# Kernel tuning notes

Hardware: AMD Instinct MI355X
Metric: run time of the kernel (lower is better)

Reference implementation:

```python
import jax, jax.numpy as jnp
import numpy as np

B, L, NW, H, HID, E, NL, DL = 32, 1024, 512, 768, 384, 4, 12, 128


def setup_inputs() -> dict:
    key = jax.random.key(0)
    ks = jax.random.split(key, 16)
    f = lambda k, s: jax.random.normal(k, s, dtype=jnp.float32) * 0.02
    z = lambda s: jnp.zeros(s, jnp.float32)
    return {
        "token_embs": jax.random.normal(ks[0], (B, L, H), dtype=jnp.float32),
        "word_maps": jnp.sort(jax.random.randint(ks[1], (B, L), 0, NW), axis=-1),
        "lang_ids": jax.random.randint(ks[2], (B,), 0, NL),
        # BiLSTM params (PyTorch gate order i,f,g,o packed along dim 0)
        "Wih_f": f(ks[3], (4 * HID, H)), "Whh_f": f(ks[4], (4 * HID, HID)),
        "bih_f": z((4 * HID,)), "bhh_f": z((4 * HID,)),
        "Wih_b": f(ks[5], (4 * HID, H)), "Whh_b": f(ks[6], (4 * HID, HID)),
        "bih_b": z((4 * HID,)), "bhh_b": z((4 * HID,)),
        "proj_W": f(ks[7], (H, 2 * HID)), "proj_b": z((H,)),
        "lang_table": f(ks[8], (NL, DL)),
        "gate_W1": f(ks[9], (H, H + DL)), "gate_b1": z((H,)),
        "gate_W2": f(ks[10], (E, H)), "gate_b2": z((E,)),
        # stacked expert heads: row i is expert i's (H,1) linear
        "ef_W": f(ks[11], (E, H)), "ef_b": z((E,)),
        "ed_W": f(ks[12], (E, H)), "ed_b": z((E,)),
    }


def _seg_mean(embs, wmap):
    # embs: [L, H], wmap: [L] -> [NW, H] per-word mean of subword embeddings
    sums = jax.ops.segment_sum(embs, wmap, num_segments=NW)
    cnt = jax.ops.segment_sum(jnp.ones(embs.shape[:1], embs.dtype), wmap, num_segments=NW)
    return sums / jnp.maximum(cnt, 1.0)[:, None]


def _lstm(x, Wih, Whh, bih, bhh, reverse):
    # x: [B, T, H] -> hidden states [B, T, HID]; gate order i,f,g,o
    def step(carry, xg):
        h, c = carry
        g = xg + h @ Whh.T + bhh
        i, fg, gg, o = jnp.split(g, 4, axis=-1)
        c = jax.nn.sigmoid(fg) * c + jax.nn.sigmoid(i) * jnp.tanh(gg)
        h = jax.nn.sigmoid(o) * jnp.tanh(c)
        return (h, c), h
    xg = jnp.swapaxes(x @ Wih.T + bih, 0, 1)  # [T, B, 4*HID], input proj hoisted
    init = (jnp.zeros((x.shape[0], Whh.shape[1]), x.dtype),) * 2
    _, hs = jax.lax.scan(step, init, xg, reverse=reverse)
    return jnp.swapaxes(hs, 0, 1)


def reference(token_embs, word_maps, lang_ids, Wih_f, Whh_f, bih_f, bhh_f,
              Wih_b, Whh_b, bih_b, bhh_b, proj_W, proj_b, lang_table,
              gate_W1, gate_b1, gate_W2, gate_b2, ef_W, ef_b, ed_W, ed_b):
    # subword -> word segment-mean pooling, batched
    word_embs = jax.vmap(_seg_mean)(token_embs, word_maps)          # [B, NW, H]
    hf = _lstm(word_embs, Wih_f, Whh_f, bih_f, bhh_f, False)        # [B, NW, HID]
    hb = _lstm(word_embs, Wih_b, Whh_b, bih_b, bhh_b, True)         # [B, NW, HID]
    seq = jnp.concatenate([hf, hb], axis=-1) @ proj_W.T + proj_b    # [B, NW, H]
    # dropout omitted (eval mode)
    gate_in = jnp.concatenate([token_embs[:, 0], lang_table[lang_ids]], axis=-1)  # [B, H+DL]
    gate = jax.nn.softmax(
        jax.nn.relu(gate_in @ gate_W1.T + gate_b1) @ gate_W2.T + gate_b2, axis=-1)  # [B, E]
    fix = jnp.einsum('bwe,be->bw', seq @ ef_W.T + ef_b, gate)       # [B, NW]
    dur = jnp.einsum('bwe,be->bw', seq @ ed_W.T + ed_b, gate)       # [B, NW]
    return (fix, dur)
```

## Files before the change

### kernel.cpp

```cpp
#include <hip/hip_runtime.h>
#include <stdint.h>

#define BB 32
#define LL 1024
#define NW 512
#define HH 768
#define HID 384
#define G4 1536
#define EE 4
#define DLL 128
#define GIN 896
#define CWG 12
#define WGC 32
#define HPAD 392

typedef __attribute__((ext_vector_type(8))) short short8;
typedef __attribute__((ext_vector_type(4))) float f32x4;
typedef __attribute__((ext_vector_type(2))) float f32x2;

__device__ __forceinline__ float bf2f(short s){
  union { unsigned int u; float f; } v; v.u = ((unsigned int)(unsigned short)s) << 16; return v.f;
}
__device__ __forceinline__ short f2bf(float f){
  union { float f; unsigned int u; } v; v.f = f;
  unsigned int r = v.u + 0x7fffu + ((v.u >> 16) & 1u);
  return (short)(r >> 16);
}
__device__ __forceinline__ float sigm(float x){ return 1.f / (1.f + __expf(-x)); }

__device__ __forceinline__ void gload16(const void* g, void* l){
  __builtin_amdgcn_global_load_lds(
      (const __attribute__((address_space(1))) unsigned int*)g,
      (__attribute__((address_space(3))) unsigned int*)l, 16, 0, 0);
}

__global__ void k_zero(int* flags, int n){
  int i = blockIdx.x * 256 + threadIdx.x;
  if (i < n) flags[i] = 0;
}

__global__ void k_f2bf(const float* in, short* out, int n){
  int i = blockIdx.x * blockDim.x + threadIdx.x;
  int st = gridDim.x * blockDim.x;
  for (; i < n; i += st) out[i] = f2bf(in[i]);
}

__global__ __launch_bounds__(256) void k_segmean(const float* __restrict__ tok,
                                                 const int* __restrict__ wmap,
                                                 short* __restrict__ we_bf){
  int blk = blockIdx.x;
  int b = blk >> 9;
  int w = blk & 511;
  const int* m = wmap + b * LL;
  int lo = 0, hi = LL;
  while (lo < hi){ int mid = (lo + hi) >> 1; if (m[mid] < w) lo = mid + 1; else hi = mid; }
  int s = lo;
  int lo2 = s, hi2 = LL;
  while (lo2 < hi2){ int mid = (lo2 + hi2) >> 1; if (m[mid] <= w) lo2 = mid + 1; else hi2 = mid; }
  int e = lo2;
  float cnt = (float)(e - s);
  float denom = fmaxf(cnt, 1.f);
  for (int j = threadIdx.x; j < HH; j += 256){
    float acc = 0.f;
    for (int r = s; r < e; ++r) acc += tok[((size_t)b * LL + r) * HH + j];
    we_bf[((size_t)b * NW + w) * HH + j] = f2bf(acc / denom);
  }
}

__global__ __launch_bounds__(256) void k_gemm_bt(const short* __restrict__ Abf,
                                                 const short* __restrict__ Wbf,
                                                 const float* __restrict__ b1,
                                                 const float* __restrict__ b2,
                                                 float* __restrict__ Cf,
                                                 int M, int N, int K){
  __shared__ __attribute__((aligned(16))) short As[128 * 32];
  __shared__ __attribute__((aligned(16))) short Bs[128 * 32];
  int ntiles = N >> 7;
  int m0 = (blockIdx.x / ntiles) << 7;
  int n0 = (blockIdx.x % ntiles) << 7;
  int tid = threadIdx.x, lane = tid & 63, wv = tid >> 6;
  int wm = (wv >> 1) << 6, wn = (wv & 1) << 6;
  f32x4 acc[4][4] = {};
  for (int kk = 0; kk < K; kk += 32){
#pragma unroll
    for (int q = 0; q < 2; ++q){
      int e = q * 256 + tid;
      int row = e >> 2, col = (e & 3) << 3;
      gload16(Abf + (size_t)(m0 + row) * K + kk + col, As + e * 8);
      gload16(Wbf + (size_t)(n0 + row) * K + kk + col, Bs + e * 8);
    }
    __syncthreads();
    short8 af[4], bfr[4];
#pragma unroll
    for (int x = 0; x < 4; ++x){
      af[x]  = *(const short8*)(As + (wm + x * 16 + (lane & 15)) * 32 + ((lane >> 4) << 3));
      bfr[x] = *(const short8*)(Bs + (wn + x * 16 + (lane & 15)) * 32 + ((lane >> 4) << 3));
    }
#pragma unroll
    for (int x = 0; x < 4; ++x)
#pragma unroll
      for (int y = 0; y < 4; ++y)
        acc[x][y] = __builtin_amdgcn_mfma_f32_16x16x32_bf16(af[x], bfr[y], acc[x][y], 0, 0, 0);
    __syncthreads();
  }
#pragma unroll
  for (int x = 0; x < 4; ++x)
#pragma unroll
    for (int y = 0; y < 4; ++y)
#pragma unroll
      for (int i = 0; i < 4; ++i){
        int mm = m0 + wm + x * 16 + ((lane >> 4) << 2) + i;
        int nn = n0 + wn + y * 16 + (lane & 15);
        Cf[(size_t)mm * N + nn] = acc[x][y][i] + b1[nn] + b2[nn];
      }
}

__global__ __launch_bounds__(512) void k_lstm(const float* __restrict__ xg_f,
                                              const float* __restrict__ xg_b,
                                              const short* __restrict__ whh_f,
                                              const short* __restrict__ whh_b,
                                              short* __restrict__ hbuf,
                                              short* __restrict__ hcat,
                                              int* __restrict__ flags){
  int bx = blockIdx.x;
  int dir = bx / CWG;
  int cg  = bx % CWG;
  int tid = threadIdx.x, lane = tid & 63, wv = tid >> 6;
  const float* xg  = dir ? xg_b : xg_f;
  const short* whh = dir ? whh_b : whh_f;
  int g  = wv >> 1;
  int nh = wv & 1;
  int jbase = g * HID + cg * WGC + nh * 16;

  short8 bfrag[12];
  {
    const short* wr = whh + (size_t)(jbase + (lane & 15)) * HID + ((lane >> 4) << 3);
#pragma unroll
    for (int ks = 0; ks < 12; ++ks) bfrag[ks] = *(const short8*)(wr + ks * 32);
  }

  __shared__ __attribute__((aligned(16))) short hs[32 * HPAD];
  __shared__ float pre[4][BB][36];

  float c0 = 0.f, c1 = 0.f;
  int eb = tid >> 4, ecp = (tid & 15) * 2;
  int pc = lane & 15;
  int* flgD = flags + dir * NW * 16;
  short* hb0 = hbuf + (size_t)dir * 2 * BB * HID;

  for (int t = 0; t < NW; ++t){
    int t_act = dir ? (NW - 1 - t) : t;
    float xgv[8];
#pragma unroll
    for (int mt = 0; mt < 2; ++mt)
#pragma unroll
      for (int i = 0; i < 4; ++i){
        int bb = mt * 16 + ((lane >> 4) << 2) + i;
        xgv[mt * 4 + i] = xg[((size_t)bb * NW + t_act) * G4 + jbase + (lane & 15)];
      }
    f32x4 acc0 = {}, acc1 = {};
    if (t > 0){
      const int* fl = flgD + (t - 1) * 16;
      for (;;){
        int v = __hip_atomic_load(&fl[pc], __ATOMIC_RELAXED, __HIP_MEMORY_SCOPE_AGENT);
        if (__all(v != 0 || pc >= CWG)) break;
      }
      const short* hp = hb0 + ((t - 1) & 1) * BB * HID;
      short8 sv0, sv1, sv2;
      {
        const short* s0 = hp + (0 * 512 + tid) * 8;
        const short* s1 = hp + (1 * 512 + tid) * 8;
        const short* s2 = hp + (2 * 512 + tid) * 8;
        asm volatile("global_load_dwordx4 %0, %1, off sc0 sc1" : "=v"(sv0) : "v"(s0) : "memory");
        asm volatile("global_load_dwordx4 %0, %1, off sc0 sc1" : "=v"(sv1) : "v"(s1) : "memory");
        asm volatile("global_load_dwordx4 %0, %1, off sc0 sc1" : "=v"(sv2) : "v"(s2) : "memory");
        asm volatile("s_waitcnt vmcnt(0)" ::: "memory");
      }
      short8 svv[3] = {sv0, sv1, sv2};
#pragma unroll
      for (int q = 0; q < 3; ++q){
        int gi = q * 512 + tid;
        int b = gi / 48, rem = gi % 48;
        *(short8*)(hs + b * HPAD + rem * 8) = svv[q];
      }
      if (cg == 0){
        int tprev = dir ? (NW - t) : (t - 1);
#pragma unroll
        for (int q = 0; q < 3; ++q){
          int gi = q * 512 + tid;
          int b = gi / 48, rem = gi % 48;
          *(short8*)(hcat + ((size_t)b * NW + tprev) * HH + dir * HID + rem * 8) = svv[q];
        }
      }
      __syncthreads();
#pragma unroll
      for (int ks = 0; ks < 12; ++ks){
        short8 a0 = *(const short8*)(hs + (lane & 15) * HPAD        + ks * 32 + ((lane >> 4) << 3));
        short8 a1 = *(const short8*)(hs + ((lane & 15) + 16) * HPAD + ks * 32 + ((lane >> 4) << 3));
        acc0 = __builtin_amdgcn_mfma_f32_16x16x32_bf16(a0, bfrag[ks], acc0, 0, 0, 0);
        acc1 = __builtin_amdgcn_mfma_f32_16x16x32_bf16(a1, bfrag[ks], acc1, 0, 0, 0);
      }
    }
#pragma unroll
    for (int i = 0; i < 4; ++i){
      int b0 = ((lane >> 4) << 2) + i;
      pre[g][b0][nh * 16 + (lane & 15)]      = acc0[i] + xgv[i];
      pre[g][b0 + 16][nh * 16 + (lane & 15)] = acc1[i] + xgv[4 + i];
    }
    __syncthreads();
    f32x2 gi2 = *(f32x2*)&pre[0][eb][ecp];
    f32x2 gf2 = *(f32x2*)&pre[1][eb][ecp];
    f32x2 gg2 = *(f32x2*)&pre[2][eb][ecp];
    f32x2 go2 = *(f32x2*)&pre[3][eb][ecp];
    c0 = sigm(gf2.x) * c0 + sigm(gi2.x) * tanhf(gg2.x);
    float h0 = sigm(go2.x) * tanhf(c0);
    c1 = sigm(gf2.y) * c1 + sigm(gi2.y) * tanhf(gg2.y);
    float h1 = sigm(go2.y) * tanhf(c1);
    unsigned int packed = (unsigned int)(unsigned short)f2bf(h0) |
                          ((unsigned int)(unsigned short)f2bf(h1) << 16);
    short* hw = hb0 + (t & 1) * BB * HID;
    __hip_atomic_store((unsigned int*)(hw + eb * HID + cg * WGC + ecp), packed,
                       __ATOMIC_RELAXED, __HIP_MEMORY_SCOPE_AGENT);
    if (t == NW - 1)
      *(unsigned int*)(hcat + ((size_t)eb * NW + t_act) * HH + dir * HID + cg * WGC + ecp) = packed;
    asm volatile("s_waitcnt vmcnt(0)" ::: "memory");
    __syncthreads();
    if (tid == 0)
      __hip_atomic_store(&flgD[t * 16 + cg], 1, __ATOMIC_RELAXED, __HIP_MEMORY_SCOPE_AGENT);
  }
}

__global__ __launch_bounds__(256) void k_gate(const float* __restrict__ tok,
                                              const int* __restrict__ lids,
                                              const float* __restrict__ ltab,
                                              const float* __restrict__ W1,
                                              const float* __restrict__ b1v,
                                              const float* __restrict__ W2,
                                              const float* __restrict__ b2v,
                                              float* __restrict__ gate){
  __shared__ float gin[GIN];
  __shared__ float hid[HH];
  __shared__ float pr[EE];
  int b = blockIdx.x, tid = threadIdx.x;
  int lid = lids[b];
  for (int i = tid; i < GIN; i += 256)
    gin[i] = (i < HH) ? tok[(size_t)b * LL * HH + i] : ltab[lid * DLL + (i - HH)];
  __syncthreads();
  for (int j = tid; j < HH; j += 256){
    float a = b1v[j];
    const float* wr = W1 + (size_t)j * GIN;
    for (int k = 0; k < GIN; ++k) a += gin[k] * wr[k];
    hid[j] = fmaxf(a, 0.f);
  }
  __syncthreads();
  int wv = tid >> 6, lane = tid & 63;
  if (wv < EE){
    float p = 0.f;
    for (int k = lane; k < HH; k += 64) p += hid[k] * W2[wv * HH + k];
#pragma unroll
    for (int off = 32; off; off >>= 1) p += __shfl_down(p, off);
    if (lane == 0) pr[wv] = p + b2v[wv];
  }
  __syncthreads();
  if (tid == 0){
    float mx = fmaxf(fmaxf(pr[0], pr[1]), fmaxf(pr[2], pr[3]));
    float s = 0.f, ex[EE];
    for (int e2 = 0; e2 < EE; ++e2){ ex[e2] = __expf(pr[e2] - mx); s += ex[e2]; }
    for (int e2 = 0; e2 < EE; ++e2) gate[b * EE + e2] = ex[e2] / s;
  }
}

__global__ __launch_bounds__(256) void k_headpre(const float* __restrict__ efW,
                                                 const float* __restrict__ efb,
                                                 const float* __restrict__ edW,
                                                 const float* __restrict__ edb,
                                                 const float* __restrict__ projW,
                                                 const float* __restrict__ projb,
                                                 float* __restrict__ Acomb,
                                                 float* __restrict__ Ccomb){
  int head = blockIdx.x >> 2, e2 = blockIdx.x & 3, tid = threadIdx.x;
  const float* Wv = head ? edW : efW;
  const float* bv = head ? edb : efb;
  __shared__ float wrow[HH];
  for (int i = tid; i < HH; i += 256) wrow[i] = Wv[e2 * HH + i];
  __syncthreads();
  for (int c = tid; c < HH; c += 256){
    float a = 0.f;
    for (int h2 = 0; h2 < HH; ++h2) a += wrow[h2] * projW[(size_t)h2 * HH + c];
    Acomb[(head * 4 + e2) * HH + c] = a;
  }
  int wv = tid >> 6, lane = tid & 63;
  if (wv == 0){
    float p = 0.f;
    for (int k = lane; k < HH; k += 64) p += wrow[k] * projb[k];
#pragma unroll
    for (int off = 32; off; off >>= 1) p += __shfl_down(p, off);
    if (lane == 0) Ccomb[head * 4 + e2] = p + bv[e2];
  }
}

__global__ __launch_bounds__(256) void k_heads(const short* __restrict__ hcat,
                                               const float* __restrict__ Acomb,
                                               const float* __restrict__ Ccomb,
                                               const float* __restrict__ gate,
                                               float* __restrict__ outp){
  __shared__ float Al[8 * HH];
  int tid = threadIdx.x;
  for (int i = tid; i < 8 * HH; i += 256) Al[i] = Acomb[i];
  __syncthreads();
  int wv = tid >> 6, lane = tid & 63;
  int bw = blockIdx.x * 4 + wv;
  const short* hr = hcat + (size_t)bw * HH;
  float hv[12];
#pragma unroll
  for (int j = 0; j < 12; ++j) hv[j] = bf2f(hr[lane + 64 * j]);
  float dsum[8];
#pragma unroll
  for (int v = 0; v < 8; ++v){
    float p = 0.f;
#pragma unroll
    for (int j = 0; j < 12; ++j) p += hv[j] * Al[v * HH + lane + 64 * j];
#pragma unroll
    for (int off = 32; off; off >>= 1) p += __shfl_xor(p, off);
    dsum[v] = p;
  }
  if (lane == 0){
    int b = bw >> 9;
    float fx = 0.f, du = 0.f;
#pragma unroll
    for (int e2 = 0; e2 < 4; ++e2){
      float g = gate[b * 4 + e2];
      fx += g * (dsum[e2]     + Ccomb[e2]);
      du += g * (dsum[4 + e2] + Ccomb[4 + e2]);
    }
    outp[bw] = fx;
    outp[BB * NW + bw] = du;
  }
}

extern "C" void kernel_launch(void* const* d_in, const int* in_sizes, int n_in,
                              void* d_out, int out_size, void* d_ws, size_t ws_size,
                              hipStream_t stream){
  const float* tok   = (const float*)d_in[0];
  const int*   wmap  = (const int*)d_in[1];
  const int*   lids  = (const int*)d_in[2];
  const float* Wih_f = (const float*)d_in[3];
  const float* Whh_f = (const float*)d_in[4];
  const float* bih_f = (const float*)d_in[5];
  const float* bhh_f = (const float*)d_in[6];
  const float* Wih_b = (const float*)d_in[7];
  const float* Whh_b = (const float*)d_in[8];
  const float* bih_b = (const float*)d_in[9];
  const float* bhh_b = (const float*)d_in[10];
  const float* projW = (const float*)d_in[11];
  const float* projb = (const float*)d_in[12];
  const float* ltab  = (const float*)d_in[13];
  const float* gW1   = (const float*)d_in[14];
  const float* gb1   = (const float*)d_in[15];
  const float* gW2   = (const float*)d_in[16];
  const float* gb2   = (const float*)d_in[17];
  const float* efW   = (const float*)d_in[18];
  const float* efb   = (const float*)d_in[19];
  const float* edW   = (const float*)d_in[20];
  const float* edb   = (const float*)d_in[21];
  float* outp = (float*)d_out;

  char* ws = (char*)d_ws;
  size_t off = 0;
  auto alloc = [&](size_t bytes) -> char* {
    char* p = ws + off;
    off = (off + bytes + 255) & ~(size_t)255;
    return p;
  };
  short* we_bf   = (short*)alloc((size_t)BB * NW * HH * 2);
  short* wihf_bf = (short*)alloc((size_t)G4 * HH * 2);
  short* wihb_bf = (short*)alloc((size_t)G4 * HH * 2);
  short* whhf_bf = (short*)alloc((size_t)G4 * HID * 2);
  short* whhb_bf = (short*)alloc((size_t)G4 * HID * 2);
  float* xg_f    = (float*)alloc((size_t)BB * NW * G4 * 4);
  float* xg_b    = (float*)alloc((size_t)BB * NW * G4 * 4);
  short* hcat    = (short*)alloc((size_t)BB * NW * HH * 2);
  short* hbuf    = (short*)alloc((size_t)2 * 2 * BB * HID * 2);
  int*   flags   = (int*)alloc((size_t)2 * NW * 16 * 4);
  float* gateb   = (float*)alloc((size_t)BB * EE * 4);
  float* Acomb   = (float*)alloc((size_t)8 * HH * 4);
  float* Ccomb   = (float*)alloc((size_t)8 * 4);

  k_zero<<<(2 * NW * 16 + 255) / 256, 256, 0, stream>>>(flags, 2 * NW * 16);
  k_f2bf<<<1024, 256, 0, stream>>>(Wih_f, wihf_bf, G4 * HH);
  k_f2bf<<<1024, 256, 0, stream>>>(Wih_b, wihb_bf, G4 * HH);
  k_f2bf<<<512, 256, 0, stream>>>(Whh_f, whhf_bf, G4 * HID);
  k_f2bf<<<512, 256, 0, stream>>>(Whh_b, whhb_bf, G4 * HID);
  k_segmean<<<BB * NW, 256, 0, stream>>>(tok, wmap, we_bf);
  k_gemm_bt<<<(BB * NW / 128) * (G4 / 128), 256, 0, stream>>>(we_bf, wihf_bf, bih_f, bhh_f, xg_f, BB * NW, G4, HH);
  k_gemm_bt<<<(BB * NW / 128) * (G4 / 128), 256, 0, stream>>>(we_bf, wihb_bf, bih_b, bhh_b, xg_b, BB * NW, G4, HH);
  k_gate<<<BB, 256, 0, stream>>>(tok, lids, ltab, gW1, gb1, gW2, gb2, gateb);
  k_headpre<<<8, 256, 0, stream>>>(efW, efb, edW, edb, projW, projb, Acomb, Ccomb);
  k_lstm<<<2 * CWG, 512, 0, stream>>>(xg_f, xg_b, whhf_bf, whhb_bf, hbuf, hcat, flags);
  k_heads<<<(BB * NW) / 4, 256, 0, stream>>>(hcat, Acomb, Ccomb, gateb, outp);
}
```

Before: 2.176 ms.

## Interleave gate columns per wave to compute LSTM cell via shuffles, drop LDS round-trip

Remaps each wave's MFMA output columns so the four i/f/g/o gates for the same hidden unit sit in adjacent lanes. The cell update then gathers them with cross-lane shuffles instead of going through a shared-memory pre-activation buffer and an extra barrier. It also splits the MFMA accumulation into two chains, uses a fast exp-based tanh, and moves the hcat writes from the cg==0 block to the owning lanes each step. Flag polling and stores now use inline-asm sc0/sc1 loads and stores. This shortens the serial per-step critical path of the recurrence, at the cost of redundant activation math and narrower 2-byte global stores.

```diff
diff --git a/kernel.cpp b/kernel.cpp
--- a/kernel.cpp
+++ b/kernel.cpp
@@ -16,7 +16,6 @@
 
 typedef __attribute__((ext_vector_type(8))) short short8;
 typedef __attribute__((ext_vector_type(4))) float f32x4;
-typedef __attribute__((ext_vector_type(2))) float f32x2;
 
 __device__ __forceinline__ float bf2f(short s){
   union { unsigned int u; float f; } v; v.u = ((unsigned int)(unsigned short)s) << 16; return v.f;
@@ -27,6 +26,12 @@
   return (short)(r >> 16);
 }
 __device__ __forceinline__ float sigm(float x){ return 1.f / (1.f + __expf(-x)); }
+__device__ __forceinline__ float ftanh(float x){ float e = __expf(2.f * x); return 1.f - 2.f / (e + 1.f); }
+__device__ __forceinline__ float pick4(int k, float v0, float v1, float v2, float v3){
+  float a = (k & 1) ? v1 : v0;
+  float b = (k & 1) ? v3 : v2;
+  return (k & 2) ? b : a;
+}
 
 __device__ __forceinline__ void gload16(const void* g, void* l){
   __builtin_amdgcn_global_load_lds(
@@ -126,43 +131,43 @@
   int dir = bx / CWG;
   int cg  = bx % CWG;
   int tid = threadIdx.x, lane = tid & 63, wv = tid >> 6;
+  int q = lane >> 4, fr = lane & 15;
+  int gate = fr >> 2, cQ = fr & 3;
+  int ncol = cg * WGC + wv * 4 + cQ;
+  int n = gate * HID + ncol;
   const float* xg  = dir ? xg_b : xg_f;
   const short* whh = dir ? whh_b : whh_f;
-  int g  = wv >> 1;
-  int nh = wv & 1;
-  int jbase = g * HID + cg * WGC + nh * 16;
 
   short8 bfrag[12];
   {
-    const short* wr = whh + (size_t)(jbase + (lane & 15)) * HID + ((lane >> 4) << 3);
+    const short* wr = whh + (size_t)n * HID + q * 8;
 #pragma unroll
     for (int ks = 0; ks < 12; ++ks) bfrag[ks] = *(const short8*)(wr + ks * 32);
   }
 
   __shared__ __attribute__((aligned(16))) short hs[32 * HPAD];
-  __shared__ float pre[4][BB][36];
-
-  float c0 = 0.f, c1 = 0.f;
-  int eb = tid >> 4, ecp = (tid & 15) * 2;
-  int pc = lane & 15;
-  int* flgD = flags + dir * NW * 16;
+
+  float cLo[4] = {0.f, 0.f, 0.f, 0.f};
+  float cHi[4] = {0.f, 0.f, 0.f, 0.f};
+  int pc = fr;
+  int* flg = flags + dir * NW * 16;
   short* hb0 = hbuf + (size_t)dir * 2 * BB * HID;
 
   for (int t = 0; t < NW; ++t){
     int t_act = dir ? (NW - 1 - t) : t;
     float xgv[8];
 #pragma unroll
-    for (int mt = 0; mt < 2; ++mt)
-#pragma unroll
-      for (int i = 0; i < 4; ++i){
-        int bb = mt * 16 + ((lane >> 4) << 2) + i;
-        xgv[mt * 4 + i] = xg[((size_t)bb * NW + t_act) * G4 + jbase + (lane & 15)];
-      }
-    f32x4 acc0 = {}, acc1 = {};
+    for (int i = 0; i < 4; ++i){
+      xgv[i]     = xg[((size_t)(q * 4 + i) * NW + t_act) * G4 + n];
+      xgv[4 + i] = xg[((size_t)(16 + q * 4 + i) * NW + t_act) * G4 + n];
+    }
+    f32x4 aL0 = {}, aL1 = {}, aH0 = {}, aH1 = {};
     if (t > 0){
-      const int* fl = flgD + (t - 1) * 16;
+      const int* fp = flg + (t - 1) * 16 + pc;
       for (;;){
-        int v = __hip_atomic_load(&fl[pc], __ATOMIC_RELAXED, __HIP_MEMORY_SCOPE_AGENT);
+        int v;
+        asm volatile("global_load_dword %0, %1, off sc0 sc1\n\ts_waitcnt vmcnt(0)"
+                     : "=v"(v) : "v"(fp) : "memory");
         if (__all(v != 0 || pc >= CWG)) break;
       }
       const short* hp = hb0 + ((t - 1) & 1) * BB * HID;
@@ -176,57 +181,70 @@
         asm volatile("global_load_dwordx4 %0, %1, off sc0 sc1" : "=v"(sv2) : "v"(s2) : "memory");
         asm volatile("s_waitcnt vmcnt(0)" ::: "memory");
       }
-      short8 svv[3] = {sv0, sv1, sv2};
-#pragma unroll
-      for (int q = 0; q < 3; ++q){
-        int gi = q * 512 + tid;
-        int b = gi / 48, rem = gi % 48;
-        *(short8*)(hs + b * HPAD + rem * 8) = svv[q];
-      }
-      if (cg == 0){
-        int tprev = dir ? (NW - t) : (t - 1);
-#pragma unroll
-        for (int q = 0; q < 3; ++q){
-          int gi = q * 512 + tid;
-          int b = gi / 48, rem = gi % 48;
-          *(short8*)(hcat + ((size_t)b * NW + tprev) * HH + dir * HID + rem * 8) = svv[q];
+      { int gi = 0 * 512 + tid; *(short8*)(hs + (gi / 48) * HPAD + (gi % 48) * 8) = sv0; }
+      { int gi = 1 * 512 + tid; *(short8*)(hs + (gi / 48) * HPAD + (gi % 48) * 8) = sv1; }
+      { int gi = 2 * 512 + tid; *(short8*)(hs + (gi / 48) * HPAD + (gi % 48) * 8) = sv2; }
+      __syncthreads();
+#pragma unroll
+      for (int ks = 0; ks < 12; ++ks){
+        short8 a0 = *(const short8*)(hs + fr * HPAD + ks * 32 + q * 8);
+        short8 a1 = *(const short8*)(hs + (fr + 16) * HPAD + ks * 32 + q * 8);
+        if (ks & 1){
+          aL1 = __builtin_amdgcn_mfma_f32_16x16x32_bf16(a0, bfrag[ks], aL1, 0, 0, 0);
+          aH1 = __builtin_amdgcn_mfma_f32_16x16x32_bf16(a1, bfrag[ks], aH1, 0, 0, 0);
+        } else {
+          aL0 = __builtin_amdgcn_mfma_f32_16x16x32_bf16(a0, bfrag[ks], aL0, 0, 0, 0);
+          aH0 = __builtin_amdgcn_mfma_f32_16x16x32_bf16(a1, bfrag[ks], aH0, 0, 0, 0);
         }
       }
-      __syncthreads();
-#pragma unroll
-      for (int ks = 0; ks < 12; ++ks){
-        short8 a0 = *(const short8*)(hs + (lane & 15) * HPAD        + ks * 32 + ((lane >> 4) << 3));
-        short8 a1 = *(const short8*)(hs + ((lane & 15) + 16) * HPAD + ks * 32 + ((lane >> 4) << 3));
-        acc0 = __builtin_amdgcn_mfma_f32_16x16x32_bf16(a0, bfrag[ks], acc0, 0, 0, 0);
-        acc1 = __builtin_amdgcn_mfma_f32_16x16x32_bf16(a1, bfrag[ks], acc1, 0, 0, 0);
-      }
-    }
+    }
+    f32x4 aLo = aL0 + aL1;
+    f32x4 aHi = aH0 + aH1;
+    unsigned int hLo[4], hHi[4];
 #pragma unroll
     for (int i = 0; i < 4; ++i){
-      int b0 = ((lane >> 4) << 2) + i;
-      pre[g][b0][nh * 16 + (lane & 15)]      = acc0[i] + xgv[i];
-      pre[g][b0 + 16][nh * 16 + (lane & 15)] = acc1[i] + xgv[4 + i];
-    }
-    __syncthreads();
-    f32x2 gi2 = *(f32x2*)&pre[0][eb][ecp];
-    f32x2 gf2 = *(f32x2*)&pre[1][eb][ecp];
-    f32x2 gg2 = *(f32x2*)&pre[2][eb][ecp];
-    f32x2 go2 = *(f32x2*)&pre[3][eb][ecp];
-    c0 = sigm(gf2.x) * c0 + sigm(gi2.x) * tanhf(gg2.x);
-    float h0 = sigm(go2.x) * tanhf(c0);
-    c1 = sigm(gf2.y) * c1 + sigm(gi2.y) * tanhf(gg2.y);
-    float h1 = sigm(go2.y) * tanhf(c1);
-    unsigned int packed = (unsigned int)(unsigned short)f2bf(h0) |
-                          ((unsigned int)(unsigned short)f2bf(h1) << 16);
+      float pl = aLo[i] + xgv[i];
+      float ph = aHi[i] + xgv[4 + i];
+      float l1 = __shfl_xor(pl, 4), l2 = __shfl_xor(pl, 8), l3 = __shfl_xor(pl, 12);
+      float m1 = __shfl_xor(ph, 4), m2 = __shfl_xor(ph, 8), m3 = __shfl_xor(ph, 12);
+      float giL = pick4(gate,     pl, l1, l2, l3);
+      float gfL = pick4(gate ^ 1, pl, l1, l2, l3);
+      float ggL = pick4(gate ^ 2, pl, l1, l2, l3);
+      float goL = pick4(gate ^ 3, pl, l1, l2, l3);
+      cLo[i] = sigm(gfL) * cLo[i] + sigm(giL) * ftanh(ggL);
+      float hL = sigm(goL) * ftanh(cLo[i]);
+      float giH = pick4(gate,     ph, m1, m2, m3);
+      float gfH = pick4(gate ^ 1, ph, m1, m2, m3);
+      float ggH = pick4(gate ^ 2, ph, m1, m2, m3);
+      float goH = pick4(gate ^ 3, ph, m1, m2, m3);
+      cHi[i] = sigm(gfH) * cHi[i] + sigm(giH) * ftanh(ggH);
+      float hH = sigm(goH) * ftanh(cHi[i]);
+      hLo[i] = (unsigned int)(unsigned short)f2bf(hL);
+      hHi[i] = (unsigned int)(unsigned short)f2bf(hH);
+    }
     short* hw = hb0 + (t & 1) * BB * HID;
-    __hip_atomic_store((unsigned int*)(hw + eb * HID + cg * WGC + ecp), packed,
-                       __ATOMIC_RELAXED, __HIP_MEMORY_SCOPE_AGENT);
-    if (t == NW - 1)
-      *(unsigned int*)(hcat + ((size_t)eb * NW + t_act) * HH + dir * HID + cg * WGC + ecp) = packed;
+    if (gate == 0){
+#pragma unroll
+      for (int i = 0; i < 4; ++i){
+        short* pL = hw + (q * 4 + i) * HID + ncol;
+        short* pH = hw + (16 + q * 4 + i) * HID + ncol;
+        asm volatile("global_store_short %0, %1, off sc0 sc1" :: "v"(pL), "v"(hLo[i]) : "memory");
+        asm volatile("global_store_short %0, %1, off sc0 sc1" :: "v"(pH), "v"(hHi[i]) : "memory");
+      }
+    } else if (gate == 1){
+#pragma unroll
+      for (int i = 0; i < 4; ++i){
+        hcat[((size_t)(q * 4 + i) * NW + t_act) * HH + dir * HID + ncol] = (short)hLo[i];
+        hcat[((size_t)(16 + q * 4 + i) * NW + t_act) * HH + dir * HID + ncol] = (short)hHi[i];
+      }
+    }
     asm volatile("s_waitcnt vmcnt(0)" ::: "memory");
     __syncthreads();
-    if (tid == 0)
-      __hip_atomic_store(&flgD[t * 16 + cg], 1, __ATOMIC_RELAXED, __HIP_MEMORY_SCOPE_AGENT);
+    if (tid == 0){
+      int one = 1;
+      int* fs = flg + t * 16 + cg;
+      asm volatile("global_store_dword %0, %1, off sc0 sc1" :: "v"(fs), "v"(one) : "memory");
+    }
   }
 }
 
@@ -386,7 +404,8 @@
   float* Acomb   = (float*)alloc((size_t)8 * HH * 4);
   float* Ccomb   = (float*)alloc((size_t)8 * 4);
 
-  k_zero<<<(2 * NW * 16 + 255) / 256, 256, 0, stream>>>(flags, 2 * NW * 16);
+  int nflag = 2 * NW * 16;
+  k_zero<<<(nflag + 255) / 256, 256, 0, stream>>>(flags, nflag);
   k_f2bf<<<1024, 256, 0, stream>>>(Wih_f, wihf_bf, G4 * HH);
   k_f2bf<<<1024, 256, 0, stream>>>(Wih_b, wihb_bf, G4 * HH);
   k_f2bf<<<512, 256, 0, stream>>>(Whh_f, whhf_bf, G4 * HID);
```

New measurement: 3.292 ms. 51.3% more time.

## Split LSTM batch into two interleaved halves to overlap sync with compute

Applied to the files above, without the earlier changes.

The persistent LSTM kernel now splits the 32-batch into two independent 16-row halves and alternates between them. Each half has its own h buffers and flags, so polling for and loading one half's hidden state overlaps with the other half's MFMA and gate math. The change also prefetches the next xg values, replaces tanhf with an exp-based tanh, writes hcat directly from every workgroup instead of only cg==0, and uses s_sleep in the spin loop. This hides the cross-workgroup barrier latency on the serial recurrence, at the cost of twice as many barrier rounds and more complex, fragile hand-ordered synchronization.

```diff
diff --git a/kernel.cpp b/kernel.cpp
--- a/kernel.cpp
+++ b/kernel.cpp
@@ -16,7 +16,6 @@
 
 typedef __attribute__((ext_vector_type(8))) short short8;
 typedef __attribute__((ext_vector_type(4))) float f32x4;
-typedef __attribute__((ext_vector_type(2))) float f32x2;
 
 __device__ __forceinline__ float bf2f(short s){
   union { unsigned int u; float f; } v; v.u = ((unsigned int)(unsigned short)s) << 16; return v.f;
@@ -27,6 +26,7 @@
   return (short)(r >> 16);
 }
 __device__ __forceinline__ float sigm(float x){ return 1.f / (1.f + __expf(-x)); }
+__device__ __forceinline__ float ftanh(float x){ float e = __expf(2.f * x); return 1.f - 2.f / (e + 1.f); }
 
 __device__ __forceinline__ void gload16(const void* g, void* l){
   __builtin_amdgcn_global_load_lds(
@@ -126,107 +126,124 @@
   int dir = bx / CWG;
   int cg  = bx % CWG;
   int tid = threadIdx.x, lane = tid & 63, wv = tid >> 6;
+  int q = lane >> 4, fr = lane & 15;
+  int g = wv >> 1, nh = wv & 1;
+  int jbase = g * HID + cg * WGC + nh * 16;
   const float* xg  = dir ? xg_b : xg_f;
   const short* whh = dir ? whh_b : whh_f;
-  int g  = wv >> 1;
-  int nh = wv & 1;
-  int jbase = g * HID + cg * WGC + nh * 16;
 
   short8 bfrag[12];
   {
-    const short* wr = whh + (size_t)(jbase + (lane & 15)) * HID + ((lane >> 4) << 3);
+    const short* wr = whh + (size_t)(jbase + fr) * HID + q * 8;
 #pragma unroll
     for (int ks = 0; ks < 12; ++ks) bfrag[ks] = *(const short8*)(wr + ks * 32);
   }
 
-  __shared__ __attribute__((aligned(16))) short hs[32 * HPAD];
-  __shared__ float pre[4][BB][36];
-
-  float c0 = 0.f, c1 = 0.f;
-  int eb = tid >> 4, ecp = (tid & 15) * 2;
-  int pc = lane & 15;
-  int* flgD = flags + dir * NW * 16;
-  short* hb0 = hbuf + (size_t)dir * 2 * BB * HID;
-
-  for (int t = 0; t < NW; ++t){
+  __shared__ __attribute__((aligned(16))) short hs[2][16 * HPAD];
+  __shared__ float pre[4][16][34];
+
+  float c0s = 0.f, c1s = 0.f;
+  int eb = tid >> 5, ecol = tid & 31;
+  int pc = fr;
+  int* flgD = flags + (size_t)dir * 2 * NW * 16;
+  short* hbD = hbuf + (size_t)dir * 2 * 2 * 16 * HID;
+
+  float xgv[4], nxg[4];
+  {
+    int t0a = dir ? (NW - 1) : 0;
+#pragma unroll
+    for (int i = 0; i < 4; ++i)
+      xgv[i] = xg[((size_t)(q * 4 + i) * NW + t0a) * G4 + jbase + fr];
+  }
+  short8 sv0, sv1;
+  int probe_v = 0;
+
+  for (int tt = 0; tt < 2 * NW; ++tt){
+    int half = tt & 1, t = tt >> 1;
     int t_act = dir ? (NW - 1 - t) : t;
-    float xgv[8];
-#pragma unroll
-    for (int mt = 0; mt < 2; ++mt)
-#pragma unroll
-      for (int i = 0; i < 4; ++i){
-        int bb = mt * 16 + ((lane >> 4) << 2) + i;
-        xgv[mt * 4 + i] = xg[((size_t)bb * NW + t_act) * G4 + jbase + (lane & 15)];
+    asm volatile("s_waitcnt vmcnt(0)" ::: "memory");
+    __builtin_amdgcn_sched_barrier(0);
+    if (tt > 0){
+#pragma unroll
+      for (int i = 0; i < 4; ++i) xgv[i] = nxg[i];
+    }
+    if (t > 0){
+      int gi0 = tid;
+      *(short8*)(&hs[half][(gi0 / 48) * HPAD + (gi0 % 48) * 8]) = sv0;
+      if (tid < 256){
+        int gi1 = 512 + tid;
+        *(short8*)(&hs[half][(gi1 / 48) * HPAD + (gi1 % 48) * 8]) = sv1;
       }
-    f32x4 acc0 = {}, acc1 = {};
+    }
+    asm volatile("s_waitcnt lgkmcnt(0)" ::: "memory");
+    __builtin_amdgcn_s_barrier();
+    __builtin_amdgcn_sched_barrier(0);
+    if (tt > 0 && tid == 0){
+      int ph = 1 - half;
+      int pt2 = (tt - 1) >> 1;
+      int one = 1;
+      int* fs = flgD + ((size_t)ph * NW + pt2) * 16 + cg;
+      asm volatile("global_store_dword %0, %1, off sc0 sc1" :: "v"(fs), "v"(one) : "memory");
+    }
+    int Y = 1 - half;
+    int tY = half ? (t + 1) : t;
+    bool do_next = (tY < NW);
+    bool do_poll = do_next && (tY > 0);
+    const int* fp = flgD + ((size_t)Y * NW + (tY - 1)) * 16 + pc;
+    if (do_poll)
+      asm volatile("global_load_dword %0, %1, off sc0 sc1" : "=v"(probe_v) : "v"(fp) : "memory");
+    f32x4 acc = {}, accB = {};
     if (t > 0){
-      const int* fl = flgD + (t - 1) * 16;
-      for (;;){
-        int v = __hip_atomic_load(&fl[pc], __ATOMIC_RELAXED, __HIP_MEMORY_SCOPE_AGENT);
-        if (__all(v != 0 || pc >= CWG)) break;
+      const short* hrow = &hs[half][fr * HPAD + q * 8];
+#pragma unroll
+      for (int ks = 0; ks < 6; ++ks)
+        acc = __builtin_amdgcn_mfma_f32_16x16x32_bf16(*(const short8*)(hrow + ks * 32), bfrag[ks], acc, 0, 0, 0);
+#pragma unroll
+      for (int ks = 6; ks < 12; ++ks)
+        accB = __builtin_amdgcn_mfma_f32_16x16x32_bf16(*(const short8*)(hrow + ks * 32), bfrag[ks], accB, 0, 0, 0);
+      acc += accB;
+    }
+#pragma unroll
+    for (int i = 0; i < 4; ++i)
+      pre[g][q * 4 + i][nh * 16 + fr] = acc[i] + xgv[i];
+    if (do_poll){
+      asm volatile("s_waitcnt vmcnt(0)" ::: "memory");
+      __builtin_amdgcn_sched_barrier(0);
+      while (!__all(probe_v != 0 || pc >= CWG)){
+        __builtin_amdgcn_s_sleep(1);
+        asm volatile("global_load_dword %0, %1, off sc0 sc1" : "=v"(probe_v) : "v"(fp) : "memory");
+        asm volatile("s_waitcnt vmcnt(0)" ::: "memory");
+        __builtin_amdgcn_sched_barrier(0);
       }
-      const short* hp = hb0 + ((t - 1) & 1) * BB * HID;
-      short8 sv0, sv1, sv2;
-      {
-        const short* s0 = hp + (0 * 512 + tid) * 8;
-        const short* s1 = hp + (1 * 512 + tid) * 8;
-        const short* s2 = hp + (2 * 512 + tid) * 8;
+    }
+    if (do_next){
+      if (tY > 0){
+        const short* hp = hbD + ((size_t)Y * 2 + ((tY - 1) & 1)) * 16 * HID;
+        const short* s0 = hp + tid * 8;
         asm volatile("global_load_dwordx4 %0, %1, off sc0 sc1" : "=v"(sv0) : "v"(s0) : "memory");
-        asm volatile("global_load_dwordx4 %0, %1, off sc0 sc1" : "=v"(sv1) : "v"(s1) : "memory");
-        asm volatile("global_load_dwordx4 %0, %1, off sc0 sc1" : "=v"(sv2) : "v"(s2) : "memory");
-        asm volatile("s_waitcnt vmcnt(0)" ::: "memory");
-      }
-      short8 svv[3] = {sv0, sv1, sv2};
-#pragma unroll
-      for (int q = 0; q < 3; ++q){
-        int gi = q * 512 + tid;
-        int b = gi / 48, rem = gi % 48;
-        *(short8*)(hs + b * HPAD + rem * 8) = svv[q];
-      }
-      if (cg == 0){
-        int tprev = dir ? (NW - t) : (t - 1);
-#pragma unroll
-        for (int q = 0; q < 3; ++q){
-          int gi = q * 512 + tid;
-          int b = gi / 48, rem = gi % 48;
-          *(short8*)(hcat + ((size_t)b * NW + tprev) * HH + dir * HID + rem * 8) = svv[q];
+        if (tid < 256){
+          const short* s1 = hp + (512 + tid) * 8;
+          asm volatile("global_load_dwordx4 %0, %1, off sc0 sc1" : "=v"(sv1) : "v"(s1) : "memory");
         }
       }
-      __syncthreads();
-#pragma unroll
-      for (int ks = 0; ks < 12; ++ks){
-        short8 a0 = *(const short8*)(hs + (lane & 15) * HPAD        + ks * 32 + ((lane >> 4) << 3));
-        short8 a1 = *(const short8*)(hs + ((lane & 15) + 16) * HPAD + ks * 32 + ((lane >> 4) << 3));
-        acc0 = __builtin_amdgcn_mfma_f32_16x16x32_bf16(a0, bfrag[ks], acc0, 0, 0, 0);
-        acc1 = __builtin_amdgcn_mfma_f32_16x16x32_bf16(a1, bfrag[ks], acc1, 0, 0, 0);
-      }
-    }
-#pragma unroll
-    for (int i = 0; i < 4; ++i){
-      int b0 = ((lane >> 4) << 2) + i;
-      pre[g][b0][nh * 16 + (lane & 15)]      = acc0[i] + xgv[i];
-      pre[g][b0 + 16][nh * 16 + (lane & 15)] = acc1[i] + xgv[4 + i];
-    }
-    __syncthreads();
-    f32x2 gi2 = *(f32x2*)&pre[0][eb][ecp];
-    f32x2 gf2 = *(f32x2*)&pre[1][eb][ecp];
-    f32x2 gg2 = *(f32x2*)&pre[2][eb][ecp];
-    f32x2 go2 = *(f32x2*)&pre[3][eb][ecp];
-    c0 = sigm(gf2.x) * c0 + sigm(gi2.x) * tanhf(gg2.x);
-    float h0 = sigm(go2.x) * tanhf(c0);
-    c1 = sigm(gf2.y) * c1 + sigm(gi2.y) * tanhf(gg2.y);
-    float h1 = sigm(go2.y) * tanhf(c1);
-    unsigned int packed = (unsigned int)(unsigned short)f2bf(h0) |
-                          ((unsigned int)(unsigned short)f2bf(h1) << 16);
-    short* hw = hb0 + (t & 1) * BB * HID;
-    __hip_atomic_store((unsigned int*)(hw + eb * HID + cg * WGC + ecp), packed,
-                       __ATOMIC_RELAXED, __HIP_MEMORY_SCOPE_AGENT);
-    if (t == NW - 1)
-      *(unsigned int*)(hcat + ((size_t)eb * NW + t_act) * HH + dir * HID + cg * WGC + ecp) = packed;
-    asm volatile("s_waitcnt vmcnt(0)" ::: "memory");
-    __syncthreads();
-    if (tid == 0)
-      __hip_atomic_store(&flgD[t * 16 + cg], 1, __ATOMIC_RELAXED, __HIP_MEMORY_SCOPE_AGENT);
+      int tYa = dir ? (NW - 1 - tY) : tY;
+#pragma unroll
+      for (int i = 0; i < 4; ++i)
+        nxg[i] = xg[((size_t)(Y * 16 + q * 4 + i) * NW + tYa) * G4 + jbase + fr];
+    }
+    asm volatile("s_waitcnt lgkmcnt(0)" ::: "memory");
+    __builtin_amdgcn_s_barrier();
+    __builtin_amdgcn_sched_barrier(0);
+    float gi2 = pre[0][eb][ecol], gf2 = pre[1][eb][ecol];
+    float gg2 = pre[2][eb][ecol], go2 = pre[3][eb][ecol];
+    float c = half ? c1s : c0s;
+    c = sigm(gf2) * c + sigm(gi2) * ftanh(gg2);
+    float h = sigm(go2) * ftanh(c);
+    if (half) c1s = c; else c0s = c;
+    unsigned int hv = (unsigned int)(unsigned short)f2bf(h);
+    short* hw = hbD + ((size_t)half * 2 + (t & 1)) * 16 * HID + eb * HID + cg * WGC + ecol;
+    asm volatile("global_store_short %0, %1, off sc0 sc1" :: "v"(hw), "v"(hv) : "memory");
+    hcat[((size_t)(half * 16 + eb) * NW + t_act) * HH + dir * HID + cg * WGC + ecol] = (short)hv;
   }
 }
 
@@ -380,13 +397,14 @@
   float* xg_f    = (float*)alloc((size_t)BB * NW * G4 * 4);
   float* xg_b    = (float*)alloc((size_t)BB * NW * G4 * 4);
   short* hcat    = (short*)alloc((size_t)BB * NW * HH * 2);
-  short* hbuf    = (short*)alloc((size_t)2 * 2 * BB * HID * 2);
-  int*   flags   = (int*)alloc((size_t)2 * NW * 16 * 4);
+  short* hbuf    = (short*)alloc((size_t)2 * 2 * 2 * 16 * HID * 2);
+  int*   flags   = (int*)alloc((size_t)2 * 2 * NW * 16 * 4);
   float* gateb   = (float*)alloc((size_t)BB * EE * 4);
   float* Acomb   = (float*)alloc((size_t)8 * HH * 4);
   float* Ccomb   = (float*)alloc((size_t)8 * 4);
 
-  k_zero<<<(2 * NW * 16 + 255) / 256, 256, 0, stream>>>(flags, 2 * NW * 16);
+  int nflag = 2 * 2 * NW * 16;
+  k_zero<<<(nflag + 255) / 256, 256, 0, stream>>>(flags, nflag);
   k_f2bf<<<1024, 256, 0, stream>>>(Wih_f, wihf_bf, G4 * HH);
   k_f2bf<<<1024, 256, 0, stream>>>(Wih_b, wihb_bf, G4 * HH);
   k_f2bf<<<512, 256, 0, stream>>>(Whh_f, whhf_bf, G4 * HID);
```

Result: slower. 2.611 ms (+20.0%).

## Replace LSTM flag handshake with tagged hidden-state words and prefetch input gates

Applied to the files above, without the earlier changes.

The recurrent LSTM kernel drops the separate per-step flag array. Each bf16 hidden value is now stored in a 32-bit word together with a 16-bit step tag, and consumers spin on the data itself until every tag matches. This removes a store-wait-barrier-flag round trip per timestep and the flag-zeroing kernel. It also prefetches the next step's input-gate values during the current step, splits the MFMA chain into two accumulators, uses an exp-based tanh, and trims one __syncthreads per step. The cost is twice the hidden-buffer traffic. Correctness now rests on tag uniqueness and on a stale buffer from an earlier launch never carrying a matching tag.

```diff
diff --git a/kernel.cpp b/kernel.cpp
--- a/kernel.cpp
+++ b/kernel.cpp
@@ -17,6 +17,8 @@
 typedef __attribute__((ext_vector_type(8))) short short8;
 typedef __attribute__((ext_vector_type(4))) float f32x4;
 typedef __attribute__((ext_vector_type(2))) float f32x2;
+typedef __attribute__((ext_vector_type(4))) unsigned int u32x4;
+typedef __attribute__((ext_vector_type(2))) unsigned int u32x2;
 
 __device__ __forceinline__ float bf2f(short s){
   union { unsigned int u; float f; } v; v.u = ((unsigned int)(unsigned short)s) << 16; return v.f;
@@ -27,16 +29,12 @@
   return (short)(r >> 16);
 }
 __device__ __forceinline__ float sigm(float x){ return 1.f / (1.f + __expf(-x)); }
+__device__ __forceinline__ float ftanh(float x){ float e = __expf(2.f * x); return 1.f - 2.f / (e + 1.f); }
 
 __device__ __forceinline__ void gload16(const void* g, void* l){
   __builtin_amdgcn_global_load_lds(
       (const __attribute__((address_space(1))) unsigned int*)g,
       (__attribute__((address_space(3))) unsigned int*)l, 16, 0, 0);
-}
-
-__global__ void k_zero(int* flags, int n){
-  int i = blockIdx.x * 256 + threadIdx.x;
-  if (i < n) flags[i] = 0;
 }
 
 __global__ void k_f2bf(const float* in, short* out, int n){
@@ -119,114 +117,147 @@
                                               const float* __restrict__ xg_b,
                                               const short* __restrict__ whh_f,
                                               const short* __restrict__ whh_b,
-                                              short* __restrict__ hbuf,
-                                              short* __restrict__ hcat,
-                                              int* __restrict__ flags){
+                                              unsigned int* __restrict__ hbuf,
+                                              short* __restrict__ hcat){
   int bx = blockIdx.x;
   int dir = bx / CWG;
   int cg  = bx % CWG;
   int tid = threadIdx.x, lane = tid & 63, wv = tid >> 6;
+  int q = lane >> 4, fr = lane & 15;
+  int g = wv >> 1, nh = wv & 1;
+  int jbase = g * HID + cg * WGC + nh * 16;
   const float* xg  = dir ? xg_b : xg_f;
   const short* whh = dir ? whh_b : whh_f;
-  int g  = wv >> 1;
-  int nh = wv & 1;
-  int jbase = g * HID + cg * WGC + nh * 16;
 
   short8 bfrag[12];
   {
-    const short* wr = whh + (size_t)(jbase + (lane & 15)) * HID + ((lane >> 4) << 3);
+    const short* wr = whh + (size_t)(jbase + fr) * HID + q * 8;
 #pragma unroll
     for (int ks = 0; ks < 12; ++ks) bfrag[ks] = *(const short8*)(wr + ks * 32);
   }
 
   __shared__ __attribute__((aligned(16))) short hs[32 * HPAD];
-  __shared__ float pre[4][BB][36];
+  __shared__ float pre[4][BB][34];
 
   float c0 = 0.f, c1 = 0.f;
   int eb = tid >> 4, ecp = (tid & 15) * 2;
-  int pc = lane & 15;
-  int* flgD = flags + dir * NW * 16;
-  short* hb0 = hbuf + (size_t)dir * 2 * BB * HID;
+  unsigned int* hbD = hbuf + (size_t)dir * 2 * BB * HID;
+  int sr = (tid * 24) / HID, sc = (tid * 24) % HID;
+
+  float xgv[8], nxg[8];
+  {
+    int t0a = dir ? (NW - 1) : 0;
+#pragma unroll
+    for (int i = 0; i < 4; ++i){
+      xgv[i]     = xg[((size_t)(q * 4 + i) * NW + t0a) * G4 + jbase + fr];
+      xgv[4 + i] = xg[((size_t)(16 + q * 4 + i) * NW + t0a) * G4 + jbase + fr];
+    }
+  }
 
   for (int t = 0; t < NW; ++t){
     int t_act = dir ? (NW - 1 - t) : t;
-    float xgv[8];
-#pragma unroll
-    for (int mt = 0; mt < 2; ++mt)
-#pragma unroll
-      for (int i = 0; i < 4; ++i){
-        int bb = mt * 16 + ((lane >> 4) << 2) + i;
-        xgv[mt * 4 + i] = xg[((size_t)bb * NW + t_act) * G4 + jbase + (lane & 15)];
-      }
-    f32x4 acc0 = {}, acc1 = {};
+    f32x4 acc0 = {}, acc1 = {}, acc0b = {}, acc1b = {};
+    u32x4 d0, d1, d2, d3, d4, d5;
     if (t > 0){
-      const int* fl = flgD + (t - 1) * 16;
+      unsigned int expect = (unsigned int)t & 0xffffu;
+      const unsigned int* hp = hbD + (size_t)((t - 1) & 1) * BB * HID + tid * 24;
       for (;;){
-        int v = __hip_atomic_load(&fl[pc], __ATOMIC_RELAXED, __HIP_MEMORY_SCOPE_AGENT);
-        if (__all(v != 0 || pc >= CWG)) break;
-      }
-      const short* hp = hb0 + ((t - 1) & 1) * BB * HID;
-      short8 sv0, sv1, sv2;
-      {
-        const short* s0 = hp + (0 * 512 + tid) * 8;
-        const short* s1 = hp + (1 * 512 + tid) * 8;
-        const short* s2 = hp + (2 * 512 + tid) * 8;
-        asm volatile("global_load_dwordx4 %0, %1, off sc0 sc1" : "=v"(sv0) : "v"(s0) : "memory");
-        asm volatile("global_load_dwordx4 %0, %1, off sc0 sc1" : "=v"(sv1) : "v"(s1) : "memory");
-        asm volatile("global_load_dwordx4 %0, %1, off sc0 sc1" : "=v"(sv2) : "v"(s2) : "memory");
+        asm volatile("global_load_dwordx4 %0, %1, off sc0 sc1" : "=v"(d0) : "v"(hp +  0) : "memory");
+        asm volatile("global_load_dwordx4 %0, %1, off sc0 sc1" : "=v"(d1) : "v"(hp +  4) : "memory");
+        asm volatile("global_load_dwordx4 %0, %1, off sc0 sc1" : "=v"(d2) : "v"(hp +  8) : "memory");
+        asm volatile("global_load_dwordx4 %0, %1, off sc0 sc1" : "=v"(d3) : "v"(hp + 12) : "memory");
+        asm volatile("global_load_dwordx4 %0, %1, off sc0 sc1" : "=v"(d4) : "v"(hp + 16) : "memory");
+        asm volatile("global_load_dwordx4 %0, %1, off sc0 sc1" : "=v"(d5) : "v"(hp + 20) : "memory");
         asm volatile("s_waitcnt vmcnt(0)" ::: "memory");
-      }
-      short8 svv[3] = {sv0, sv1, sv2};
-#pragma unroll
-      for (int q = 0; q < 3; ++q){
-        int gi = q * 512 + tid;
-        int b = gi / 48, rem = gi % 48;
-        *(short8*)(hs + b * HPAD + rem * 8) = svv[q];
-      }
+        __builtin_amdgcn_sched_barrier(0);
+#define TAGBAD(dv) (((dv[0] ^ expect) | (dv[1] ^ expect) | (dv[2] ^ expect) | (dv[3] ^ expect)) & 0xffffu)
+        unsigned int bad = TAGBAD(d0) | TAGBAD(d1) | TAGBAD(d2) | TAGBAD(d3) | TAGBAD(d4) | TAGBAD(d5);
+#undef TAGBAD
+        if (__all(bad == 0)) break;
+        __builtin_amdgcn_s_sleep(1);
+      }
+      unsigned int pk0  = (d0[0] >> 16) | (d0[1] & 0xffff0000u);
+      unsigned int pk1  = (d0[2] >> 16) | (d0[3] & 0xffff0000u);
+      unsigned int pk2  = (d1[0] >> 16) | (d1[1] & 0xffff0000u);
+      unsigned int pk3  = (d1[2] >> 16) | (d1[3] & 0xffff0000u);
+      unsigned int pk4  = (d2[0] >> 16) | (d2[1] & 0xffff0000u);
+      unsigned int pk5  = (d2[2] >> 16) | (d2[3] & 0xffff0000u);
+      unsigned int pk6  = (d3[0] >> 16) | (d3[1] & 0xffff0000u);
+      unsigned int pk7  = (d3[2] >> 16) | (d3[3] & 0xffff0000u);
+      unsigned int pk8  = (d4[0] >> 16) | (d4[1] & 0xffff0000u);
+      unsigned int pk9  = (d4[2] >> 16) | (d4[3] & 0xffff0000u);
+      unsigned int pk10 = (d5[0] >> 16) | (d5[1] & 0xffff0000u);
+      unsigned int pk11 = (d5[2] >> 16) | (d5[3] & 0xffff0000u);
+      u32x4 P0 = {pk0, pk1, pk2, pk3};
+      u32x4 P1 = {pk4, pk5, pk6, pk7};
+      u32x4 P2 = {pk8, pk9, pk10, pk11};
+      short* dst = hs + sr * HPAD + sc;
+      *(u32x4*)(dst)      = P0;
+      *(u32x4*)(dst + 8)  = P1;
+      *(u32x4*)(dst + 16) = P2;
       if (cg == 0){
         int tprev = dir ? (NW - t) : (t - 1);
-#pragma unroll
-        for (int q = 0; q < 3; ++q){
-          int gi = q * 512 + tid;
-          int b = gi / 48, rem = gi % 48;
-          *(short8*)(hcat + ((size_t)b * NW + tprev) * HH + dir * HID + rem * 8) = svv[q];
-        }
-      }
-      __syncthreads();
-#pragma unroll
-      for (int ks = 0; ks < 12; ++ks){
-        short8 a0 = *(const short8*)(hs + (lane & 15) * HPAD        + ks * 32 + ((lane >> 4) << 3));
-        short8 a1 = *(const short8*)(hs + ((lane & 15) + 16) * HPAD + ks * 32 + ((lane >> 4) << 3));
-        acc0 = __builtin_amdgcn_mfma_f32_16x16x32_bf16(a0, bfrag[ks], acc0, 0, 0, 0);
-        acc1 = __builtin_amdgcn_mfma_f32_16x16x32_bf16(a1, bfrag[ks], acc1, 0, 0, 0);
-      }
+        short* dh = hcat + ((size_t)sr * NW + tprev) * HH + dir * HID + sc;
+        *(u32x4*)(dh)      = P0;
+        *(u32x4*)(dh + 8)  = P1;
+        *(u32x4*)(dh + 16) = P2;
+      }
+#pragma unroll
+      for (int i = 0; i < 8; ++i) xgv[i] = nxg[i];
+    }
+    asm volatile("s_waitcnt lgkmcnt(0)" ::: "memory");
+    __builtin_amdgcn_s_barrier();
+    __builtin_amdgcn_sched_barrier(0);
+    if (t + 1 < NW){
+      int tn = dir ? (NW - 2 - t) : (t + 1);
+#pragma unroll
+      for (int i = 0; i < 4; ++i){
+        nxg[i]     = xg[((size_t)(q * 4 + i) * NW + tn) * G4 + jbase + fr];
+        nxg[4 + i] = xg[((size_t)(16 + q * 4 + i) * NW + tn) * G4 + jbase + fr];
+      }
+    }
+    if (t > 0){
+      const short* hrow0 = hs + fr * HPAD + q * 8;
+      const short* hrow1 = hs + (fr + 16) * HPAD + q * 8;
+#pragma unroll
+      for (int ks = 0; ks < 6; ++ks){
+        acc0  = __builtin_amdgcn_mfma_f32_16x16x32_bf16(*(const short8*)(hrow0 + ks * 32), bfrag[ks], acc0, 0, 0, 0);
+        acc1  = __builtin_amdgcn_mfma_f32_16x16x32_bf16(*(const short8*)(hrow1 + ks * 32), bfrag[ks], acc1, 0, 0, 0);
+      }
+#pragma unroll
+      for (int ks = 6; ks < 12; ++ks){
+        acc0b = __builtin_amdgcn_mfma_f32_16x16x32_bf16(*(const short8*)(hrow0 + ks * 32), bfrag[ks], acc0b, 0, 0, 0);
+        acc1b = __builtin_amdgcn_mfma_f32_16x16x32_bf16(*(const short8*)(hrow1 + ks * 32), bfrag[ks], acc1b, 0, 0, 0);
+      }
+      acc0 += acc0b; acc1 += acc1b;
     }
 #pragma unroll
     for (int i = 0; i < 4; ++i){
-      int b0 = ((lane >> 4) << 2) + i;
-      pre[g][b0][nh * 16 + (lane & 15)]      = acc0[i] + xgv[i];
-      pre[g][b0 + 16][nh * 16 + (lane & 15)] = acc1[i] + xgv[4 + i];
-    }
-    __syncthreads();
+      int b0 = q * 4 + i;
+      pre[g][b0][nh * 16 + fr]      = acc0[i] + xgv[i];
+      pre[g][b0 + 16][nh * 16 + fr] = acc1[i] + xgv[4 + i];
+    }
+    asm volatile("s_waitcnt lgkmcnt(0)" ::: "memory");
+    __builtin_amdgcn_s_barrier();
+    __builtin_amdgcn_sched_barrier(0);
     f32x2 gi2 = *(f32x2*)&pre[0][eb][ecp];
     f32x2 gf2 = *(f32x2*)&pre[1][eb][ecp];
     f32x2 gg2 = *(f32x2*)&pre[2][eb][ecp];
     f32x2 go2 = *(f32x2*)&pre[3][eb][ecp];
-    c0 = sigm(gf2.x) * c0 + sigm(gi2.x) * tanhf(gg2.x);
-    float h0 = sigm(go2.x) * tanhf(c0);
-    c1 = sigm(gf2.y) * c1 + sigm(gi2.y) * tanhf(gg2.y);
-    float h1 = sigm(go2.y) * tanhf(c1);
-    unsigned int packed = (unsigned int)(unsigned short)f2bf(h0) |
-                          ((unsigned int)(unsigned short)f2bf(h1) << 16);
-    short* hw = hb0 + (t & 1) * BB * HID;
-    __hip_atomic_store((unsigned int*)(hw + eb * HID + cg * WGC + ecp), packed,
-                       __ATOMIC_RELAXED, __HIP_MEMORY_SCOPE_AGENT);
-    if (t == NW - 1)
-      *(unsigned int*)(hcat + ((size_t)eb * NW + t_act) * HH + dir * HID + cg * WGC + ecp) = packed;
-    asm volatile("s_waitcnt vmcnt(0)" ::: "memory");
-    __syncthreads();
-    if (tid == 0)
-      __hip_atomic_store(&flgD[t * 16 + cg], 1, __ATOMIC_RELAXED, __HIP_MEMORY_SCOPE_AGENT);
+    c0 = sigm(gf2.x) * c0 + sigm(gi2.x) * ftanh(gg2.x);
+    float h0 = sigm(go2.x) * ftanh(c0);
+    c1 = sigm(gf2.y) * c1 + sigm(gi2.y) * ftanh(gg2.y);
+    float h1 = sigm(go2.y) * ftanh(c1);
+    unsigned int us0 = (unsigned int)(unsigned short)f2bf(h0);
+    unsigned int us1 = (unsigned int)(unsigned short)f2bf(h1);
+    unsigned int tagw = (unsigned int)(t + 1) & 0xffffu;
+    u32x2 wvx = {(us0 << 16) | tagw, (us1 << 16) | tagw};
+    unsigned int* hw = hbD + (size_t)(t & 1) * BB * HID + eb * HID + cg * WGC + ecp;
+    asm volatile("global_store_dwordx2 %0, %1, off sc0 sc1" :: "v"(hw), "v"(wvx) : "memory");
+    if (t == NW - 1){
+      unsigned int hc = us0 | (us1 << 16);
+      *(unsigned int*)(hcat + ((size_t)eb * NW + t_act) * HH + dir * HID + cg * WGC + ecp) = hc;
+    }
   }
 }
 
@@ -380,13 +411,11 @@
   float* xg_f    = (float*)alloc((size_t)BB * NW * G4 * 4);
   float* xg_b    = (float*)alloc((size_t)BB * NW * G4 * 4);
   short* hcat    = (short*)alloc((size_t)BB * NW * HH * 2);
-  short* hbuf    = (short*)alloc((size_t)2 * 2 * BB * HID * 2);
-  int*   flags   = (int*)alloc((size_t)2 * NW * 16 * 4);
+  unsigned int* hbuf = (unsigned int*)alloc((size_t)2 * 2 * BB * HID * 4);
   float* gateb   = (float*)alloc((size_t)BB * EE * 4);
   float* Acomb   = (float*)alloc((size_t)8 * HH * 4);
   float* Ccomb   = (float*)alloc((size_t)8 * 4);
 
-  k_zero<<<(2 * NW * 16 + 255) / 256, 256, 0, stream>>>(flags, 2 * NW * 16);
   k_f2bf<<<1024, 256, 0, stream>>>(Wih_f, wihf_bf, G4 * HH);
   k_f2bf<<<1024, 256, 0, stream>>>(Wih_b, wihb_bf, G4 * HH);
   k_f2bf<<<512, 256, 0, stream>>>(Whh_f, whhf_bf, G4 * HID);
@@ -396,6 +425,6 @@
   k_gemm_bt<<<(BB * NW / 128) * (G4 / 128), 256, 0, stream>>>(we_bf, wihb_bf, bih_b, bhh_b, xg_b, BB * NW, G4, HH);
   k_gate<<<BB, 256, 0, stream>>>(tok, lids, ltab, gW1, gb1, gW2, gb2, gateb);
   k_headpre<<<8, 256, 0, stream>>>(efW, efb, edW, edb, projW, projb, Acomb, Ccomb);
-  k_lstm<<<2 * CWG, 512, 0, stream>>>(xg_f, xg_b, whhf_bf, whhb_bf, hbuf, hcat, flags);
+  k_lstm<<<2 * CWG, 512, 0, stream>>>(xg_f, xg_b, whhf_bf, whhb_bf, hbuf, hcat);
   k_heads<<<(BB * NW) / 4, 256, 0, stream>>>(hcat, Acomb, Ccomb, gateb, outp);
 }
```

After: 3.165 ms. 45.5% more time.
